# Kernel optimization log

Measured on AMD Instinct MI355X. Metric: run time of the kernel, lower is better.

The kernel has to match this reference:

```python
import jax, jax.numpy as jnp
import numpy as np

X_DIM, XC_DIM, G_DIM = 45, 10, 20
P_DIM = XC_DIM * G_DIM  # 200
N_ITER, KAPPA, LAMDA, YITA = 5, 0.8, 0.9999, 0.5
B = 131072


def _mlp(h, W1, b1, W2, b2):
    # MLP(in,out) with activation=(elu, None): elu hidden, linear out
    return jax.nn.elu(h @ W1 + b1) @ W2 + b2


def _f_p(h):
    # hippocampal nonlinearity: leaky_relu clamped to [-1, 1]
    return jnp.clip(jax.nn.leaky_relu(h), -1.0, 1.0)


def _retrieve(q, M0):
    # iterative Hopfield-like attractor retrieval (n_iteration fixed, small)
    p = q
    for _ in range(N_ITER):
        p = _f_p(KAPPA * p + p @ M0)
    return p


def setup_inputs() -> dict:
    key = jax.random.key(0)
    ks = jax.random.split(key, 12)
    s = 0.1  # small param scale for numerical sanity
    return {
        "x": jax.random.normal(ks[0], (B, X_DIM), jnp.float32),
        "g": jax.random.normal(ks[1], (B, G_DIM), jnp.float32),
        # M buffer starts at zeros in the module; use small noise so retrieval is nontrivial
        "M": 0.01 * jax.random.normal(ks[2], (1, P_DIM, P_DIM), jnp.float32),
        "W_comp": s * jax.random.normal(ks[3], (X_DIM, XC_DIM), jnp.float32),
        "W1_ie": s * jax.random.normal(ks[4], (G_DIM, 2 * G_DIM), jnp.float32),
        "b1_ie": jnp.zeros((2 * G_DIM,), jnp.float32),
        "W2_ie": s * jax.random.normal(ks[5], (2 * G_DIM, G_DIM), jnp.float32),
        "b2_ie": jnp.zeros((G_DIM,), jnp.float32),
        "W1_gg": s * jax.random.normal(ks[6], (G_DIM, 2 * G_DIM), jnp.float32),
        "b1_gg": jnp.zeros((2 * G_DIM,), jnp.float32),
        "W2_gg": s * jax.random.normal(ks[7], (2 * G_DIM, G_DIM), jnp.float32),
        "b2_gg": jnp.zeros((G_DIM,), jnp.float32),
        "W_sp": s * jax.random.normal(ks[8], (XC_DIM, X_DIM), jnp.float32),
        "b_sp": jnp.zeros((X_DIM,), jnp.float32),
    }


def reference(x, g, M, W_comp, W1_ie, b1_ie, W2_ie, b2_ie,
              W1_gg, b1_gg, W2_gg, b2_gg, W_sp, b_sp):
    # fixed structural matrices (buffers in torch)
    W_tile = jnp.kron(jnp.ones((1, G_DIM), jnp.float32), jnp.eye(XC_DIM, dtype=jnp.float32))   # [xc, p]
    W_repeat = jnp.kron(jnp.eye(G_DIM, dtype=jnp.float32), jnp.ones((1, XC_DIM), jnp.float32))  # [g, p]
    M0 = M[0]

    # compress sensory -> hippocampal sensory component
    xc = x @ W_comp                 # [B, xc]
    x_ = xc @ W_tile                # [B, p]

    # retrieve from memory with sensory cue, infer entorhinal g
    px = _retrieve(x_, M0)          # [B, p]
    g_inf = jnp.clip(_mlp(px @ W_repeat.T, W1_ie, b1_ie, W2_ie, b2_ie), -1.0, 1.0)  # [B, g]

    # path integration / entorhinal transition, project to hippocampus
    g2 = jnp.tanh(_mlp(g, W1_gg, b1_gg, W2_gg, b2_gg))  # [B, g]
    g_ = g2 @ W_repeat              # [B, p]

    # retrieve with entorhinal cue, predict sensory observation
    p = _retrieve(g_, M0)           # [B, p]
    x_inf = (p @ W_tile.T) @ W_sp + b_sp  # [B, x]

    # inferred hippocampal state (conjunction) and Hebbian memory update
    p_inf = _f_p(g_ * x_)           # [B, p]
    hebb = ((p_inf - p).T @ (p_inf + p)) / jnp.asarray(x.shape[0], x.dtype)  # [p, p]
    M_new = LAMDA * M + YITA * hebb[None]

    return (g_inf, x_inf, g_, x_, M_new)
```

## Files before the change

### kernel.cpp

```cpp
#include <hip/hip_runtime.h>

#define B_TOTAL 131072
#define PD 200
#define KAPPA 0.8f
#define LAMDA 0.9999f
#define YITA 0.5f
#define MS_KS 216
#define HB_RS 72

typedef short short8 __attribute__((ext_vector_type(8)));
typedef short short4v __attribute__((ext_vector_type(4)));
typedef float f32x16 __attribute__((ext_vector_type(16)));
typedef unsigned uint4v __attribute__((ext_vector_type(4)));

static __device__ __forceinline__ float bf2f(unsigned short h) {
  union { unsigned u; float f; } v; v.u = ((unsigned)h) << 16; return v.f;
}
static __device__ __forceinline__ unsigned short f2bf(float f) {
  union { float f; unsigned u; } v; v.f = f;
  unsigned r = v.u + 0x7FFFu + ((v.u >> 16) & 1u);
  return (unsigned short)(r >> 16);
}
static __device__ __forceinline__ float fp_nl(float v) {
  float t = fmaxf(v, 0.01f * v);
  return fminf(1.f, fmaxf(-1.f, t));
}
static __device__ __forceinline__ unsigned pkbf(float lo, float hi) {
  unsigned r;
  asm("v_cvt_pk_bf16_f32 %0, %1, %2" : "=v"(r) : "v"(lo), "v"(hi));
  return r;
}
static __device__ __forceinline__ void swap32(unsigned &a, unsigned &b) {
  asm("s_nop 1\n\tv_permlane32_swap_b32 %0, %1" : "+v"(a), "+v"(b));
}
static __device__ __forceinline__ uint4v mk4(unsigned a, unsigned b, unsigned c, unsigned d) {
  uint4v v; v[0] = a; v[1] = b; v[2] = c; v[3] = d; return v;
}
static __device__ __forceinline__ short8 u4s8(uint4v w) {
  union { uint4v u; short8 s; } x; x.u = w; return x.s;
}

__global__ void tem_init_m(const float* __restrict__ Min, float* __restrict__ oM) {
  int i = blockIdx.x * 256 + threadIdx.x;
  if (i < PD * PD) oM[i] = LAMDA * Min[i];
}

__global__ __launch_bounds__(256, 4) void tem_pre(
    const float* __restrict__ xin, const float* __restrict__ gin,
    const float* __restrict__ Wc,
    const float* __restrict__ W1gg, const float* __restrict__ b1gg,
    const float* __restrict__ W2gg, const float* __restrict__ b2gg,
    float* __restrict__ o_g, float* __restrict__ o_x) {
  __shared__ unsigned short xcS[128 * 10];
  __shared__ float g2S[128 * 20];
  const int tid = threadIdx.x;
  const int r0 = blockIdx.x * 128;

  if (tid < 128) {
    const int rq = r0 + tid;
    float gv[20];
#pragma unroll
    for (int i = 0; i < 20; ++i) gv[i] = gin[(size_t)rq * 20 + i];
    float out20[20];
#pragma unroll
    for (int o = 0; o < 20; ++o) out20[o] = b2gg[o];
#pragma unroll 1
    for (int u = 0; u < 40; ++u) {
      float hu = b1gg[u];
#pragma unroll
      for (int i = 0; i < 20; ++i) hu += gv[i] * W1gg[i * 40 + u];
      hu = (hu > 0.f) ? hu : (expf(hu) - 1.f);
#pragma unroll
      for (int o = 0; o < 20; ++o) out20[o] += hu * W2gg[u * 20 + o];
    }
#pragma unroll
    for (int o = 0; o < 20; ++o) g2S[tid * 20 + o] = tanhf(out20[o]);
  } else {
    const int rr2 = tid - 128;
    const int rq = r0 + rr2;
    float xc[10];
#pragma unroll
    for (int o = 0; o < 10; ++o) xc[o] = 0.f;
#pragma unroll 1
    for (int j = 0; j < 45; ++j) {
      const float xv = xin[(size_t)rq * 45 + j];
#pragma unroll
      for (int o = 0; o < 10; ++o) xc[o] += xv * Wc[j * 10 + o];
    }
#pragma unroll
    for (int o = 0; o < 10; ++o) xcS[rr2 * 10 + o] = f2bf(xc[o]);
  }
  __syncthreads();
  for (int i = tid; i < 128 * 200; i += 256) {
    const int rP = i / 200, j = i - rP * 200;
    o_g[(size_t)(r0 + rP) * 200 + j] = g2S[rP * 20 + j / 10];
    o_x[(size_t)(r0 + rP) * 200 + j] = bf2f(xcS[rP * 10 + (j % 10)]);
  }
}

#define LDMS(nt, kc) (*(const short8*)(Ms + (((nt) * 32 + cl) * MS_KS + (kc) * 16 + hi * 8)))
#define MFMA_AG(ACC, A, B) asm("v_mfma_f32_32x32x16_bf16 %0, %1, %2, %0" : "+a"(ACC) : "v"(A), "v"(B))

#define STEP(PF, KC) do { \
  const short8 _b = u4s8(PF); \
  { const short8 _a = LDMS(0, KC); MFMA_AG(acc0, _a, _b); } \
  { const short8 _a = LDMS(1, KC); MFMA_AG(acc1, _a, _b); } \
  { const short8 _a = LDMS(2, KC); MFMA_AG(acc2, _a, _b); } \
  { const short8 _a = LDMS(3, KC); MFMA_AG(acc3, _a, _b); } \
  { const short8 _a = LDMS(4, KC); MFMA_AG(acc4, _a, _b); } \
  { const short8 _a = LDMS(5, KC); MFMA_AG(acc5, _a, _b); } \
  { const short8 _a = LDMS(6, KC); MFMA_AG(acc6, _a, _b); } \
} while (0)

#define REPACK_LO(ACC, PF) do { \
  unsigned P0 = pkbf(fp_nl(ACC[0]), fp_nl(ACC[1])); \
  unsigned P1 = pkbf(fp_nl(ACC[2]), fp_nl(ACC[3])); \
  unsigned P2 = pkbf(fp_nl(ACC[4]), fp_nl(ACC[5])); \
  unsigned P3 = pkbf(fp_nl(ACC[6]), fp_nl(ACC[7])); \
  swap32(P0, P2); swap32(P1, P3); \
  PF = mk4(P0, P1, P2, P3); \
} while (0)
#define REPACK_HI(ACC, PF) do { \
  unsigned P4 = pkbf(fp_nl(ACC[8]),  fp_nl(ACC[9])); \
  unsigned P5 = pkbf(fp_nl(ACC[10]), fp_nl(ACC[11])); \
  unsigned P6 = pkbf(fp_nl(ACC[12]), fp_nl(ACC[13])); \
  unsigned P7 = pkbf(fp_nl(ACC[14]), fp_nl(ACC[15])); \
  swap32(P4, P6); swap32(P5, P7); \
  PF = mk4(P4, P5, P6, P7); \
} while (0)

#define ITER5 do { \
  f32x16 acc0 = {}, acc1 = {}, acc2 = {}, acc3 = {}, acc4 = {}, acc5 = {}, acc6 = {}; \
  STEP(pfA0, 0);  STEP(pfA1, 1);  STEP(pfA2, 2);  STEP(pfA3, 3); \
  STEP(pfA4, 4);  STEP(pfA5, 5);  STEP(pfA6, 6);  STEP(pfA7, 7); \
  STEP(pfA8, 8);  STEP(pfA9, 9);  STEP(pfA10, 10); STEP(pfA11, 11); \
  STEP(pfA12, 12); \
  REPACK_LO(acc0, pfA0);  REPACK_HI(acc0, pfA1); \
  REPACK_LO(acc1, pfA2);  REPACK_HI(acc1, pfA3); \
  REPACK_LO(acc2, pfA4);  REPACK_HI(acc2, pfA5); \
  REPACK_LO(acc3, pfA6);  REPACK_HI(acc3, pfA7); \
  REPACK_LO(acc4, pfA8);  REPACK_HI(acc4, pfA9); \
  REPACK_LO(acc5, pfA10); REPACK_HI(acc5, pfA11); \
  REPACK_LO(acc6, pfA12); \
} while (0)

#define FORR_LO(M_) M_(pfA0,0) M_(pfA1,16) M_(pfA2,32) M_(pfA3,48) M_(pfA4,64) M_(pfA5,80) \
                    M_(pfA6,96) M_(pfA7,112) M_(pfA8,128) M_(pfA9,144) M_(pfA10,160) M_(pfA11,176) M_(pfA12,192)
#define FORR_HI(M_) M_(pfA0,8) M_(pfA1,24) M_(pfA2,40) M_(pfA3,56) M_(pfA4,72) M_(pfA5,88) \
                    M_(pfA6,104) M_(pfA7,120) M_(pfA8,136) M_(pfA9,152) M_(pfA10,168) M_(pfA11,184)

#define INX(PF, BB) PF = mk4( \
  pkbf(xcv[((BB) + 0) % 10], xcv[((BB) + 1) % 10]), \
  pkbf(xcv[((BB) + 2) % 10], xcv[((BB) + 3) % 10]), \
  pkbf(xcv[((BB) + 4) % 10], xcv[((BB) + 5) % 10]), \
  pkbf(xcv[((BB) + 6) % 10], xcv[((BB) + 7) % 10]));
#define ING(PF, BB) PF = mk4( \
  pkbf(g2v[((BB) + 0) / 10], g2v[((BB) + 1) / 10]), \
  pkbf(g2v[((BB) + 2) / 10], g2v[((BB) + 3) / 10]), \
  pkbf(g2v[((BB) + 4) / 10], g2v[((BB) + 5) / 10]), \
  pkbf(g2v[((BB) + 6) / 10], g2v[((BB) + 7) / 10]));

#define E1W(W, F) { bins[(F) / 10] += bf2f((unsigned short)((W) & 0xFFFFu)); \
                    bins[((F) + 1) / 10] += bf2f((unsigned short)((W) >> 16)); }
#define E1PF(PF, BB) { E1W(PF[0], (BB) + 0) E1W(PF[1], (BB) + 2) E1W(PF[2], (BB) + 4) E1W(PF[3], (BB) + 6) }

#define E2AW(W, F) { ta[(F) % 10] += bf2f((unsigned short)((W) & 0xFFFFu)); \
                     ta[((F) + 1) % 10] += bf2f((unsigned short)((W) >> 16)); }
#define E2APF(PF, BB) { E2AW(PF[0], (BB) + 0) E2AW(PF[1], (BB) + 2) E2AW(PF[2], (BB) + 4) E2AW(PF[3], (BB) + 6) }

#define STG(PF, SL) (((uint4v*)StgRaw)[(wid * 4 + (SL)) * 64 + lane] = PF)

__global__ __launch_bounds__(512, 1) void tem_main(
    const float* __restrict__ xin, const float* __restrict__ gin,
    const float* __restrict__ Min, const float* __restrict__ Wc,
    const float* __restrict__ W1ie, const float* __restrict__ b1ie,
    const float* __restrict__ W2ie, const float* __restrict__ b2ie,
    const float* __restrict__ W1gg, const float* __restrict__ b1gg,
    const float* __restrict__ W2gg, const float* __restrict__ b2gg,
    const float* __restrict__ Wsp, const float* __restrict__ bsp,
    float* __restrict__ o_ginf, float* __restrict__ o_xinf,
    unsigned short* __restrict__ dWp, unsigned short* __restrict__ sWp) {
  __shared__ __attribute__((aligned(16))) unsigned short Ms[224 * MS_KS];
  __shared__ unsigned short xcS[256 * 10];
  __shared__ float g2S[256 * 20];
  __shared__ __attribute__((aligned(16))) char StgRaw[32768];

  unsigned* StgU = (unsigned*)StgRaw;
  float* StgF = (float*)StgRaw;

  const int tid = threadIdx.x;
  const int lane = tid & 63;
  const int wid = tid >> 6;
  const int cl = lane & 31;
  const int hi = lane >> 5;
  const int r0 = blockIdx.x * 256;

  {
    unsigned* Ms32 = (unsigned*)Ms;
    for (int i = tid; i < 224 * MS_KS / 2; i += 512) Ms32[i] = 0u;
  }
  __syncthreads();
  for (int i = tid; i < 200 * 224; i += 512) {
    const int k = i / 224, n = i - k * 224;
    if (n < 200) {
      float v = Min[k * 200 + n];
      if (k == n) v += KAPPA;
      Ms[n * MS_KS + k] = f2bf(v);
    }
  }

  if (tid < 256) {
    const int rq = r0 + tid;
    float gv[20];
#pragma unroll
    for (int i = 0; i < 20; ++i) gv[i] = gin[(size_t)rq * 20 + i];
    float h[40];
#pragma unroll
    for (int u = 0; u < 40; ++u) h[u] = b1gg[u];
#pragma unroll
    for (int i = 0; i < 20; ++i)
#pragma unroll
      for (int u = 0; u < 40; ++u) h[u] += gv[i] * W1gg[i * 40 + u];
#pragma unroll
    for (int u = 0; u < 40; ++u) h[u] = (h[u] > 0.f) ? h[u] : (expf(h[u]) - 1.f);
#pragma unroll
    for (int o = 0; o < 20; ++o) {
      float v = b2gg[o];
#pragma unroll
      for (int u = 0; u < 40; ++u) v += h[u] * W2gg[u * 20 + o];
      g2S[tid * 20 + o] = tanhf(v);
    }
  } else {
    const int rr2 = tid - 256;
    const int rq = r0 + rr2;
    float xc[10];
#pragma unroll
    for (int o = 0; o < 10; ++o) xc[o] = 0.f;
#pragma unroll 1
    for (int j = 0; j < 45; ++j) {
      const float xv = xin[(size_t)rq * 45 + j];
#pragma unroll
      for (int o = 0; o < 10; ++o) xc[o] += xv * Wc[j * 10 + o];
    }
#pragma unroll
    for (int o = 0; o < 10; ++o) xcS[rr2 * 10 + o] = f2bf(xc[o]);
  }
  __syncthreads();

  const int rr = wid * 32 + cl;
  const int r = r0 + rr;

  uint4v pfA0, pfA1, pfA2, pfA3, pfA4, pfA5, pfA6, pfA7, pfA8, pfA9, pfA10, pfA11, pfA12;

  {
    float xcv[10];
#pragma unroll
    for (int o = 0; o < 10; ++o) xcv[o] = bf2f(xcS[rr * 10 + o]);
    if (hi == 0) { FORR_LO(INX) }
    else         { FORR_HI(INX) pfA12 = mk4(0u, 0u, 0u, 0u); }
  }
#pragma unroll 1
  for (int it = 0; it < 5; ++it) { ITER5; }
  {
    float bins[20];
#pragma unroll
    for (int t = 0; t < 20; ++t) bins[t] = 0.f;
    if (hi == 0) { FORR_LO(E1PF) } else { FORR_HI(E1PF) }
#pragma unroll
    for (int t = 0; t < 20; ++t) bins[t] += __shfl_xor(bins[t], 32);
    float h[40];
#pragma unroll
    for (int u = 0; u < 40; ++u) h[u] = b1ie[u];
#pragma unroll
    for (int gg = 0; gg < 20; ++gg) {
      const float bv = bins[gg];
#pragma unroll
      for (int u = 0; u < 40; ++u) h[u] += bv * W1ie[gg * 40 + u];
    }
#pragma unroll
    for (int u = 0; u < 40; ++u) h[u] = (h[u] > 0.f) ? h[u] : (expf(h[u]) - 1.f);
#pragma unroll
    for (int oi = 0; oi < 10; ++oi) {
      const int o = hi * 10 + oi;
      float v = b2ie[o];
#pragma unroll
      for (int u = 0; u < 40; ++u) v += h[u] * W2ie[u * 20 + o];
      StgF[rr * 20 + o] = fminf(1.f, fmaxf(-1.f, v));
    }
  }
  __syncthreads();
  for (int i = tid; i < 256 * 20; i += 512) o_ginf[(size_t)r0 * 20 + i] = StgF[i];
  __syncthreads();

  {
    float g2v[20];
#pragma unroll
    for (int o = 0; o < 20; ++o) g2v[o] = g2S[rr * 20 + o];
    if (hi == 0) { FORR_LO(ING) }
    else         { FORR_HI(ING) pfA12 = mk4(0u, 0u, 0u, 0u); }
  }
#pragma unroll 1
  for (int it = 0; it < 5; ++it) { ITER5; }
  {
    float ta[10];
#pragma unroll
    for (int t = 0; t < 10; ++t) ta[t] = 0.f;
    if (hi == 0) { FORR_LO(E2APF) } else { FORR_HI(E2APF) }
#pragma unroll
    for (int t = 0; t < 10; ++t) ta[t] += __shfl_xor(ta[t], 32);
#pragma unroll 1
    for (int ph = 0; ph < 2; ++ph) {
      if ((rr >> 7) == ph) {
        const int rL = rr & 127;
        const int o0 = hi ? 23 : 0, o1 = hi ? 45 : 23;
#pragma unroll 1
        for (int o = o0; o < o1; ++o) {
          float v = bsp[o];
#pragma unroll
          for (int a = 0; a < 10; ++a) v += ta[a] * Wsp[a * 45 + o];
          StgF[rL * 45 + o] = v;
        }
      }
      __syncthreads();
      for (int i = tid; i < 128 * 45; i += 512)
        o_xinf[((size_t)r0 + ph * 128) * 45 + i] = StgF[i];
      __syncthreads();
    }
  }
  {
    unsigned int* dW32 = (unsigned int*)dWp;
    unsigned int* sW32 = (unsigned int*)sWp;
#pragma unroll 1
    for (int rnd = 0; rnd < 4; ++rnd) {
      if (rnd == 0)      { STG(pfA0, 0);  STG(pfA1, 1);  STG(pfA2, 2);   STG(pfA3, 3);  }
      else if (rnd == 1) { STG(pfA4, 0);  STG(pfA5, 1);  STG(pfA6, 2);   STG(pfA7, 3);  }
      else if (rnd == 2) { STG(pfA8, 0);  STG(pfA9, 1);  STG(pfA10, 2);  STG(pfA11, 3); }
      else               { STG(pfA12, 0); }
      asm volatile("s_waitcnt lgkmcnt(0)" ::: "memory");
      __builtin_amdgcn_sched_barrier(0);
#pragma unroll 1
      for (int itw = 0; itw < 16; ++itw) {
        const int idx = itw * 64 + lane;
        const int row = idx >> 5;
        const int jpo = idx & 31;
        const int jp = rnd * 32 + jpo;
        if (jp < 100) {
          const int kcl = jpo >> 3, rem = jpo & 7;
          const int hi2 = rem >> 2, jw = rem & 3;
          const unsigned word = StgU[(((wid * 4 + kcl) * 2 + hi2) * 32 + row) * 4 + jw];
          const int rB = wid * 32 + row;
          const int j0 = jp * 2;
          const float p0 = bf2f((unsigned short)(word & 0xFFFFu));
          const float p1 = bf2f((unsigned short)(word >> 16));
          const float x0 = bf2f(xcS[rB * 10 + (j0 % 10)]);
          const float x1 = bf2f(xcS[rB * 10 + ((j0 + 1) % 10)]);
          const float pi0 = fp_nl(g2S[rB * 20 + (j0 / 10)] * x0);
          const float pi1 = fp_nl(g2S[rB * 20 + ((j0 + 1) / 10)] * x1);
          const unsigned dpack = (unsigned)f2bf(pi0 - p0) | ((unsigned)f2bf(pi1 - p1) << 16);
          const unsigned spack = (unsigned)f2bf(pi0 + p0) | ((unsigned)f2bf(pi1 + p1) << 16);
          const size_t oidx = (size_t)(r0 + rB) * 100 + jp;
          dW32[oidx] = dpack;
          sW32[oidx] = spack;
        }
      }
      __builtin_amdgcn_sched_barrier(0);
    }
  }
}

__global__ __launch_bounds__(448, 1) void tem_hebb(
    const unsigned short* __restrict__ dWp, const unsigned short* __restrict__ sWp,
    float* __restrict__ oM) {
  __shared__ __attribute__((aligned(16))) unsigned short dT[224 * HB_RS];
  __shared__ __attribute__((aligned(16))) unsigned short sT[224 * HB_RS];
  const int tid = threadIdx.x;
  const int lane = tid & 63, wid = tid >> 6;
  const int cl = lane & 31, hi = lane >> 5;
  for (int i = tid; i < 224 * HB_RS; i += 448) { dT[i] = 0; sT[i] = 0; }
  f32x16 hacc[7];
#pragma unroll
  for (int nt = 0; nt < 7; ++nt)
#pragma unroll
    for (int q = 0; q < 16; ++q) hacc[nt][q] = 0.f;
  const int kbase = blockIdx.x * 512;
#pragma unroll 1
  for (int sub = 0; sub < 8; ++sub) {
    __syncthreads();
    const int kb = kbase + sub * 64;
#pragma unroll 1
    for (int i = tid; i < 64 * 50; i += 448) {
      const int rr = i / 50, fq = i - rr * 50;
      const int f0 = fq * 4;
      const short4v d4 = *(const short4v*)(dWp + ((size_t)(kb + rr) * 200 + f0));
      const short4v s4 = *(const short4v*)(sWp + ((size_t)(kb + rr) * 200 + f0));
#pragma unroll
      for (int q = 0; q < 4; ++q) {
        dT[(f0 + q) * HB_RS + rr] = (unsigned short)d4[q];
        sT[(f0 + q) * HB_RS + rr] = (unsigned short)s4[q];
      }
    }
    __syncthreads();
#pragma unroll
    for (int kc = 0; kc < 4; ++kc) {
      const short8 af = *(const short8*)(dT + ((wid * 32 + cl) * HB_RS + kc * 16 + hi * 8));
#pragma unroll
      for (int nt = 0; nt < 7; ++nt) {
        const short8 bfr = *(const short8*)(sT + ((nt * 32 + cl) * HB_RS + kc * 16 + hi * 8));
        hacc[nt] = __builtin_amdgcn_mfma_f32_32x32x16_bf16(af, bfr, hacc[nt], 0, 0, 0);
      }
    }
  }
  const float scale = YITA / (float)B_TOTAL;
#pragma unroll
  for (int nt = 0; nt < 7; ++nt) {
    const int j = nt * 32 + cl;
    if (j < 200) {
#pragma unroll
      for (int rg = 0; rg < 16; ++rg) {
        const int ii = wid * 32 + (rg & 3) + 8 * (rg >> 2) + 4 * hi;
        if (ii < 200) atomicAdd(&oM[ii * 200 + j], hacc[nt][rg] * scale);
      }
    }
  }
}

extern "C" void kernel_launch(void* const* d_in, const int* in_sizes, int n_in,
                              void* d_out, int out_size, void* d_ws, size_t ws_size,
                              hipStream_t stream) {
  (void)in_sizes; (void)n_in; (void)out_size; (void)ws_size;
  const float* xin  = (const float*)d_in[0];
  const float* gin  = (const float*)d_in[1];
  const float* Min  = (const float*)d_in[2];
  const float* Wc   = (const float*)d_in[3];
  const float* W1ie = (const float*)d_in[4];
  const float* b1ie = (const float*)d_in[5];
  const float* W2ie = (const float*)d_in[6];
  const float* b2ie = (const float*)d_in[7];
  const float* W1gg = (const float*)d_in[8];
  const float* b1gg = (const float*)d_in[9];
  const float* W2gg = (const float*)d_in[10];
  const float* b2gg = (const float*)d_in[11];
  const float* Wsp  = (const float*)d_in[12];
  const float* bsp  = (const float*)d_in[13];

  float* out = (float*)d_out;
  float* o_ginf = out;
  float* o_xinf = out + (size_t)B_TOTAL * 20;
  float* o_g    = out + (size_t)B_TOTAL * 65;
  float* o_x    = out + (size_t)B_TOTAL * 265;
  float* o_M    = out + (size_t)B_TOTAL * 465;

  unsigned short* dWp = (unsigned short*)d_ws;
  unsigned short* sWp = dWp + (size_t)B_TOTAL * PD;

  tem_init_m<<<(PD * PD + 255) / 256, 256, 0, stream>>>(Min, o_M);
  tem_pre<<<1024, 256, 0, stream>>>(xin, gin, Wc, W1gg, b1gg, W2gg, b2gg, o_g, o_x);
  tem_main<<<512, 512, 0, stream>>>(xin, gin, Min, Wc, W1ie, b1ie, W2ie, b2ie,
                                    W1gg, b1gg, W2gg, b2gg, Wsp, bsp,
                                    o_ginf, o_xinf, dWp, sWp);
  tem_hebb<<<256, 448, 0, stream>>>(dWp, sWp, o_M);
}
```

Before: 516.6 us.

## Store hebbian difference/sum buffers in column-chunked layout and add sched barrier in MFMA step

Changes the intermediate bf16 d/s buffers from row-major [B,200] to a chunked layout of three 64-column planes plus an 8-column tail plane. The writer loop skips the wasted idle lanes of the last round, and each warp's stores now form contiguous 128-byte segments. The hebb kernel reads through a matching index helper. A sched_barrier is also added after each MFMA step, which constrains how the compiler interleaves instructions in the retrieval loop.

```diff
diff --git a/kernel.cpp b/kernel.cpp
--- a/kernel.cpp
+++ b/kernel.cpp
@@ -38,6 +38,13 @@
 }
 static __device__ __forceinline__ short8 u4s8(uint4v w) {
   union { uint4v u; short8 s; } x; x.u = w; return x.s;
+}
+
+static __device__ __forceinline__ short4v ld4ds(const unsigned short* p, int r, int f0) {
+  const size_t off = (f0 < 192)
+      ? ((size_t)(f0 >> 6) * B_TOTAL + (size_t)r) * 64 + (f0 & 63)
+      : (size_t)3 * B_TOTAL * 64 + (size_t)r * 8 + (f0 - 192);
+  return *(const short4v*)(p + off);
 }
 
 __global__ void tem_init_m(const float* __restrict__ Min, float* __restrict__ oM) {
@@ -110,6 +117,7 @@
   { const short8 _a = LDMS(4, KC); MFMA_AG(acc4, _a, _b); } \
   { const short8 _a = LDMS(5, KC); MFMA_AG(acc5, _a, _b); } \
   { const short8 _a = LDMS(6, KC); MFMA_AG(acc6, _a, _b); } \
+  __builtin_amdgcn_sched_barrier(0); \
 } while (0)
 
 #define REPACK_LO(ACC, PF) do { \
@@ -338,17 +346,16 @@
       else               { STG(pfA12, 0); }
       asm volatile("s_waitcnt lgkmcnt(0)" ::: "memory");
       __builtin_amdgcn_sched_barrier(0);
-#pragma unroll 1
-      for (int itw = 0; itw < 16; ++itw) {
-        const int idx = itw * 64 + lane;
-        const int row = idx >> 5;
-        const int jpo = idx & 31;
-        const int jp = rnd * 32 + jpo;
-        if (jp < 100) {
+      if (rnd < 3) {
+#pragma unroll 1
+        for (int itw = 0; itw < 16; ++itw) {
+          const int u = itw * 64 + lane;
+          const int row = u >> 5, jpo = u & 31;
           const int kcl = jpo >> 3, rem = jpo & 7;
           const int hi2 = rem >> 2, jw = rem & 3;
           const unsigned word = StgU[(((wid * 4 + kcl) * 2 + hi2) * 32 + row) * 4 + jw];
           const int rB = wid * 32 + row;
+          const int jp = rnd * 32 + jpo;
           const int j0 = jp * 2;
           const float p0 = bf2f((unsigned short)(word & 0xFFFFu));
           const float p1 = bf2f((unsigned short)(word >> 16));
@@ -358,7 +365,27 @@
           const float pi1 = fp_nl(g2S[rB * 20 + ((j0 + 1) / 10)] * x1);
           const unsigned dpack = (unsigned)f2bf(pi0 - p0) | ((unsigned)f2bf(pi1 - p1) << 16);
           const unsigned spack = (unsigned)f2bf(pi0 + p0) | ((unsigned)f2bf(pi1 + p1) << 16);
-          const size_t oidx = (size_t)(r0 + rB) * 100 + jp;
+          const size_t oidx = ((size_t)rnd * B_TOTAL + (size_t)(r0 + rB)) * 32 + jpo;
+          dW32[oidx] = dpack;
+          sW32[oidx] = spack;
+        }
+      } else {
+#pragma unroll 1
+        for (int itw = 0; itw < 2; ++itw) {
+          const int u = itw * 64 + lane;
+          const int row = u >> 2, q = u & 3;
+          const unsigned word = StgU[((wid * 8) * 32 + row) * 4 + q];
+          const int rB = wid * 32 + row;
+          const int j0 = (96 + q) * 2;
+          const float p0 = bf2f((unsigned short)(word & 0xFFFFu));
+          const float p1 = bf2f((unsigned short)(word >> 16));
+          const float x0 = bf2f(xcS[rB * 10 + (j0 % 10)]);
+          const float x1 = bf2f(xcS[rB * 10 + ((j0 + 1) % 10)]);
+          const float pi0 = fp_nl(g2S[rB * 20 + (j0 / 10)] * x0);
+          const float pi1 = fp_nl(g2S[rB * 20 + ((j0 + 1) / 10)] * x1);
+          const unsigned dpack = (unsigned)f2bf(pi0 - p0) | ((unsigned)f2bf(pi1 - p1) << 16);
+          const unsigned spack = (unsigned)f2bf(pi0 + p0) | ((unsigned)f2bf(pi1 + p1) << 16);
+          const size_t oidx = (size_t)3 * B_TOTAL * 32 + (size_t)(r0 + rB) * 4 + q;
           dW32[oidx] = dpack;
           sW32[oidx] = spack;
         }
@@ -391,8 +418,8 @@
     for (int i = tid; i < 64 * 50; i += 448) {
       const int rr = i / 50, fq = i - rr * 50;
       const int f0 = fq * 4;
-      const short4v d4 = *(const short4v*)(dWp + ((size_t)(kb + rr) * 200 + f0));
-      const short4v s4 = *(const short4v*)(sWp + ((size_t)(kb + rr) * 200 + f0));
+      const short4v d4 = ld4ds(dWp, kb + rr, f0);
+      const short4v s4 = ld4ds(sWp, kb + rr, f0);
 #pragma unroll
       for (int q = 0; q < 4; ++q) {
         dT[(f0 + q) * HB_RS + rr] = (unsigned short)d4[q];
```

New measurement: 489.9 us. -5.2%, faster.
